# Kernel optimization log

Hardware: AMD Instinct MI355X
Metric: run time of the kernel (lower is better)

## Reference

```python
import jax, jax.numpy as jnp
import numpy as np

TAU = 0.5
LOGIT_TAU = float(np.log(TAU / (1.0 - TAU)))  # = 0.0 for tau=0.5
N_STEPS = 128           # torch samples randint(128,129) -> always 128
N_SECANT = 8
D_MIN, D_MAX = 0.0, 2.4
B, N, HID, CDIM = 4, 8192, 64, 128


def decoder(p, c, W1, Wc, b1, W2, b2):
    """Occupancy-logit MLP. p: (B, ..., 3), c: (B, CDIM) -> (B, ...)."""
    cc = c @ Wc  # (B, HID)
    cc = cc.reshape(cc.shape[:1] + (1,) * (p.ndim - 2) + cc.shape[1:])
    h = jax.nn.relu(jnp.einsum('...d,dh->...h', p, W1) + cc + b1)
    return (h @ W2 + b2)[..., 0]


def setup_inputs() -> dict:
    key = jax.random.key(0)
    ks = jax.random.split(key, 8)
    return {
        'ray0': jax.random.normal(ks[0], (B, N, 3), jnp.float32) * 0.5,
        'ray_direction': jax.random.normal(ks[1], (B, N, 3), jnp.float32),
        'c': jax.random.normal(ks[2], (B, CDIM), jnp.float32),
        'W1': jax.random.normal(ks[3], (3, HID), jnp.float32) * 0.5,
        'Wc': jax.random.normal(ks[4], (CDIM, HID), jnp.float32) * 0.1,
        'b1': jax.random.normal(ks[5], (HID,), jnp.float32) * 0.1,
        'W2': jax.random.normal(ks[6], (HID, 1), jnp.float32) * 0.5,
        'b2': jax.random.normal(ks[7], (1,), jnp.float32) * 0.1,
    }


def reference(ray0, ray_direction, c, W1, Wc, b1, W2, b2):
    S = N_STEPS
    bsz, npts, _ = ray0.shape
    dec = lambda p: decoder(p, c, W1, Wc, b1, W2, b2)

    # --- coarse ray marching ---
    d_prop = jnp.linspace(D_MIN, D_MAX, S).astype(ray0.dtype)        # (S,)
    p_prop = ray0[:, :, None, :] + ray_direction[:, :, None, :] * d_prop[None, None, :, None]
    val = dec(p_prop) - LOGIT_TAU                                    # (B, N, S)

    mask_0_not_occupied = val[:, :, 0] < 0
    sign_matrix = jnp.concatenate(
        [jnp.sign(val[:, :, :-1] * val[:, :, 1:]),
         jnp.ones((bsz, npts, 1), val.dtype)], axis=-1)
    cost_matrix = sign_matrix * jnp.arange(S, 0, -1, dtype=val.dtype)
    indices = jnp.argmin(cost_matrix, axis=-1)                       # (B, N)
    values = jnp.min(cost_matrix, axis=-1)
    mask_sign_change = values < 0
    f_low = jnp.take_along_axis(val, indices[..., None], axis=2)[..., 0]
    mask_neg_to_pos = f_low < 0
    mask = mask_sign_change & mask_neg_to_pos & mask_0_not_occupied

    d_prop_full = jnp.broadcast_to(d_prop, (bsz, npts, S))
    d_low = jnp.take_along_axis(d_prop_full, indices[..., None], axis=2)[..., 0]
    idx_hi = jnp.minimum(indices + 1, S - 1)
    d_high = jnp.take_along_axis(d_prop_full, idx_hi[..., None], axis=2)[..., 0]
    f_high = jnp.take_along_axis(val, idx_hi[..., None], axis=2)[..., 0]

    # safe placeholders for non-surface rays (results discarded by mask)
    d_low = jnp.where(mask, d_low, 0.0)
    d_high = jnp.where(mask, d_high, 1.0)
    f_low = jnp.where(mask, f_low, -1.0)
    f_high = jnp.where(mask, f_high, 1.0)

    # --- secant refinement (vectorized over all rays) ---
    d_pred = -f_low * (d_high - d_low) / (f_high - f_low) + d_low
    for _ in range(N_SECANT):
        p_mid = ray0 + d_pred[..., None] * ray_direction
        f_mid = dec(p_mid) - LOGIT_TAU
        ind_low = f_mid < 0
        d_low = jnp.where(ind_low, d_pred, d_low)
        f_low = jnp.where(ind_low, f_mid, f_low)
        d_high = jnp.where(ind_low, d_high, d_pred)
        f_high = jnp.where(ind_low, f_high, f_mid)
        d_pred = -f_low * (d_high - d_low) / (f_high - f_low) + d_low

    d_out = jnp.where(mask, d_pred, jnp.inf)
    d_out = jnp.where(mask_0_not_occupied, d_out, 0.0)
    return d_out
```

## Files before the change

### kernel.cpp

```cpp
#include <hip/hip_runtime.h>
#include <hip/hip_bf16.h>

#define HID   64
#define CDIM  128
#define NSTEP 128
#define NRAYS 32768

typedef const __hip_bfloat16* __restrict__ bf16p;
typedef float v2f __attribute__((ext_vector_type(2)));

__device__ __forceinline__ float bf2f(__hip_bfloat16 x) { return __bfloat162float(x); }

#if __has_builtin(__builtin_elementwise_fma)
__device__ __forceinline__ v2f vfma2(v2f a, v2f b, v2f c) { return __builtin_elementwise_fma(a, b, c); }
#else
__device__ __forceinline__ v2f vfma2(v2f a, v2f b, v2f c) {
    v2f r; r.x = fmaf(a.x, b.x, c.x); r.y = fmaf(a.y, b.y, c.y); return r;
}
#endif
#if __has_builtin(__builtin_elementwise_max)
__device__ __forceinline__ v2f vmax2(v2f a, v2f b) { return __builtin_elementwise_max(a, b); }
#else
__device__ __forceinline__ v2f vmax2(v2f a, v2f b) {
    v2f r; r.x = fmaxf(a.x, b.x); r.y = fmaxf(a.y, b.y); return r;
}
#endif
__device__ __forceinline__ v2f splat2(float s) { v2f v; v.x = s; v.y = s; return v; }

__global__ void precompute_cc(bf16p c, bf16p Wc, bf16p b1, float* __restrict__ ccb1) {
    __shared__ float part[4][HID];
    int b = blockIdx.x;
    int h = threadIdx.x & 63;
    int q = threadIdx.x >> 6;
    float acc = 0.0f;
    const __hip_bfloat16* crow = c + b * CDIM;
#pragma unroll
    for (int k = q * 32; k < q * 32 + 32; ++k)
        acc = fmaf(bf2f(crow[k]), bf2f(Wc[k * HID + h]), acc);
    part[q][h] = acc;
    __syncthreads();
    if (q == 0)
        ccb1[b * HID + h] = bf2f(b1[h]) + ((part[0][h] + part[1][h]) + (part[2][h] + part[3][h]));
}

__global__ __launch_bounds__(256) void raymarch(
    bf16p ray0, bf16p rdir, bf16p W1, bf16p W2, bf16p b2,
    const float* __restrict__ ccb1, __hip_bfloat16* __restrict__ out) {
    __shared__ float4 sWX[HID / 4], sWY[HID / 4], sWZ[HID / 4], sW2[HID / 4], sCB[HID / 4];

    const int tid  = threadIdx.x;
    const int wave = tid >> 6;
    const int lane = tid & 63;
    const int r    = blockIdx.x * 4 + wave;
    const int batch = blockIdx.x >> 11;

    if (tid < HID) {
        ((float*)sWX)[tid] = bf2f(W1[tid]);
        ((float*)sWY)[tid] = bf2f(W1[HID + tid]);
        ((float*)sWZ)[tid] = bf2f(W1[2 * HID + tid]);
        ((float*)sW2)[tid] = bf2f(W2[tid]);
        ((float*)sCB)[tid] = ccb1[batch * HID + tid];
    }
    __syncthreads();

    const float b2v = bf2f(b2[0]);
    const float ox = bf2f(ray0[r * 3 + 0]), oy = bf2f(ray0[r * 3 + 1]), oz = bf2f(ray0[r * 3 + 2]);
    const float dx = bf2f(rdir[r * 3 + 0]), dy = bf2f(rdir[r * 3 + 1]), dz = bf2f(rdir[r * 3 + 2]);

    const float STEPF = 2.4f / 127.0f;
    const float d0 = bf2f(__float2bfloat16(lane * STEPF));
    const float d1 = bf2f(__float2bfloat16((lane + 64) * STEPF));

    v2f dv; dv.x = d0; dv.y = d1;
    const v2f pxv = vfma2(dv, splat2(dx), splat2(ox));
    const v2f pyv = vfma2(dv, splat2(dy), splat2(oy));
    const v2f pzv = vfma2(dv, splat2(dz), splat2(oz));

    v2f acc = splat2(b2v);
    const v2f zero2 = splat2(0.0f);
#pragma unroll
    for (int g = 0; g < HID / 4; ++g) {
        const float4 wx4 = sWX[g], wy4 = sWY[g], wz4 = sWZ[g], w24 = sW2[g], cb4 = sCB[g];
        const float* wx = (const float*)&wx4;
        const float* wy = (const float*)&wy4;
        const float* wz = (const float*)&wz4;
        const float* w2 = (const float*)&w24;
        const float* cb = (const float*)&cb4;
#pragma unroll
        for (int jj = 0; jj < 4; ++jj) {
            v2f h = vfma2(pxv, splat2(wx[jj]),
                    vfma2(pyv, splat2(wy[jj]),
                    vfma2(pzv, splat2(wz[jj]), splat2(cb[jj]))));
            h = vmax2(h, zero2);
            acc = vfma2(h, splat2(w2[jj]), acc);
        }
    }
    float val0 = acc.x, val1 = acc.y;

    float v1l0  = __shfl(val1, 0);
    float valn0 = __shfl_down(val0, 1);
    valn0 = (lane == 63) ? v1l0 : valn0;
    float valn1 = __shfl_down(val1, 1);

    float prod0 = val0 * valn0;
    float sgn0  = (prod0 < 0.0f) ? -1.0f : ((prod0 > 0.0f) ? 1.0f : 0.0f);
    float cost0 = sgn0 * (float)(128 - lane);

    float prod1 = val1 * valn1;
    float sgn1  = (prod1 < 0.0f) ? -1.0f : ((prod1 > 0.0f) ? 1.0f : 0.0f);
    float cost1 = (lane == 63) ? 1.0f
                               : sgn1 * (float)(64 - lane);

    float key0 = fmaf(cost0, 256.0f, (float)lane);
    float key1 = fmaf(cost1, 256.0f, (float)(lane + 64));
    float k = fminf(key0, key1);
#pragma unroll
    for (int off = 32; off > 0; off >>= 1)
        k = fminf(k, __shfl_xor(k, off));
    const float cf = floorf(k * 0.00390625f);
    const int   mi = (int)(k - cf * 256.0f);

    const int idx  = mi;
    const int idxh = (idx + 1 < NSTEP) ? idx + 1 : NSTEP - 1;

    float va  = __shfl(val0, idx  & 63);
    float vb  = __shfl(val1, idx  & 63);
    float f_low  = (idx  < 64) ? va  : vb;
    float vah = __shfl(val0, idxh & 63);
    float vbh = __shfl(val1, idxh & 63);
    float f_high = (idxh < 64) ? vah : vbh;

    float v00 = __shfl(val0, 0);
    bool  m0   = v00 < 0.0f;
    bool  mask = (cf < 0.0f) && (f_low < 0.0f) && m0;

    float result;
    if (mask) {
        float dl = bf2f(__float2bfloat16(idx  * STEPF));
        float dh = bf2f(__float2bfloat16(idxh * STEPF));
        float fl = f_low, fh = f_high;
        const float wlx = ((const float*)sWX)[lane];
        const float wly = ((const float*)sWY)[lane];
        const float wlz = ((const float*)sWZ)[lane];
        const float wl2 = ((const float*)sW2)[lane];
        const float cbl = ((const float*)sCB)[lane];
        float dp = -fl * (dh - dl) / (fh - fl) + dl;
#pragma unroll
        for (int it = 0; it < 8; ++it) {
            float px = fmaf(dp, dx, ox), py = fmaf(dp, dy, oy), pz = fmaf(dp, dz, oz);
            float h = fmaf(px, wlx, fmaf(py, wly, fmaf(pz, wlz, cbl)));
            h = fmaxf(h, 0.0f);
            float t = h * wl2;
            for (int off = 32; off > 0; off >>= 1) t += __shfl_xor(t, off);
            float fm = t + b2v;
            bool lowside = fm < 0.0f;
            dl = lowside ? dp : dl;
            fl = lowside ? fm : fl;
            dh = lowside ? dh : dp;
            fh = lowside ? fh : fm;
            dp = -fl * (dh - dl) / (fh - fl) + dl;
        }
        result = dp;
    } else {
        result = m0 ? 0x1.FEp127f : 0.0f;
    }
    if (lane == 0) out[r] = __float2bfloat16(result);
}

extern "C" void kernel_launch(void* const* d_in, const int* in_sizes, int n_in,
                              void* d_out, int out_size, void* d_ws, size_t ws_size,
                              hipStream_t stream) {
    bf16p ray0 = (bf16p)d_in[0];
    bf16p rdir = (bf16p)d_in[1];
    bf16p c    = (bf16p)d_in[2];
    bf16p W1   = (bf16p)d_in[3];
    bf16p Wc   = (bf16p)d_in[4];
    bf16p b1   = (bf16p)d_in[5];
    bf16p W2   = (bf16p)d_in[6];
    bf16p b2   = (bf16p)d_in[7];
    __hip_bfloat16* out = (__hip_bfloat16*)d_out;
    float* ccb1 = (float*)d_ws;

    hipLaunchKernelGGL(precompute_cc, dim3(4), dim3(256), 0, stream, c, Wc, b1, ccb1);
    hipLaunchKernelGGL(raymarch, dim3(NRAYS / 4), dim3(256), 0, stream,
                       ray0, rdir, W1, W2, b2, ccb1, out);
}
```

Measured before the change: 100.4 us.

## Preconvert MLP weights to fp32 workspace and drop shared-memory staging

The precompute kernel now also converts W1 and W2 to fp32 in the workspace. The raymarch kernel reads weights directly from global memory (uniform, cacheable loads) instead of staging them in LDS behind a __syncthreads. The inner MLP loop is also restructured to vectorize over hidden units in pairs rather than over the two sample points, which needs a final horizontal add. This removes per-block bf16 conversion and the barrier, at the cost of relying on scalar/global cache loads for the weights.

```diff
diff --git a/kernel.cpp b/kernel.cpp
--- a/kernel.cpp
+++ b/kernel.cpp
@@ -8,6 +8,12 @@
 
 typedef const __hip_bfloat16* __restrict__ bf16p;
 typedef float v2f __attribute__((ext_vector_type(2)));
+
+#define WS_CCB 0
+#define WS_WX  256
+#define WS_WY  320
+#define WS_WZ  384
+#define WS_W2  448
 
 __device__ __forceinline__ float bf2f(__hip_bfloat16 x) { return __bfloat162float(x); }
 
@@ -27,7 +33,8 @@
 #endif
 __device__ __forceinline__ v2f splat2(float s) { v2f v; v.x = s; v.y = s; return v; }
 
-__global__ void precompute_cc(bf16p c, bf16p Wc, bf16p b1, float* __restrict__ ccb1) {
+__global__ void precompute_cc(bf16p c, bf16p Wc, bf16p b1, bf16p W1, bf16p W2,
+                              float* __restrict__ ws) {
     __shared__ float part[4][HID];
     int b = blockIdx.x;
     int h = threadIdx.x & 63;
@@ -38,30 +45,35 @@
     for (int k = q * 32; k < q * 32 + 32; ++k)
         acc = fmaf(bf2f(crow[k]), bf2f(Wc[k * HID + h]), acc);
     part[q][h] = acc;
+    if (b == 0) {
+        if (q == 1) {
+            ws[WS_WX + h] = bf2f(W1[h]);
+            ws[WS_WY + h] = bf2f(W1[HID + h]);
+        } else if (q == 2) {
+            ws[WS_WZ + h] = bf2f(W1[2 * HID + h]);
+            ws[WS_W2 + h] = bf2f(W2[h]);
+        }
+    }
     __syncthreads();
     if (q == 0)
-        ccb1[b * HID + h] = bf2f(b1[h]) + ((part[0][h] + part[1][h]) + (part[2][h] + part[3][h]));
+        ws[WS_CCB + b * HID + h] =
+            bf2f(b1[h]) + ((part[0][h] + part[1][h]) + (part[2][h] + part[3][h]));
 }
 
 __global__ __launch_bounds__(256) void raymarch(
-    bf16p ray0, bf16p rdir, bf16p W1, bf16p W2, bf16p b2,
-    const float* __restrict__ ccb1, __hip_bfloat16* __restrict__ out) {
-    __shared__ float4 sWX[HID / 4], sWY[HID / 4], sWZ[HID / 4], sW2[HID / 4], sCB[HID / 4];
-
+    bf16p ray0, bf16p rdir, bf16p b2,
+    const float* __restrict__ ws, __hip_bfloat16* __restrict__ out) {
     const int tid  = threadIdx.x;
     const int wave = tid >> 6;
     const int lane = tid & 63;
     const int r    = blockIdx.x * 4 + wave;
     const int batch = blockIdx.x >> 11;
 
-    if (tid < HID) {
-        ((float*)sWX)[tid] = bf2f(W1[tid]);
-        ((float*)sWY)[tid] = bf2f(W1[HID + tid]);
-        ((float*)sWZ)[tid] = bf2f(W1[2 * HID + tid]);
-        ((float*)sW2)[tid] = bf2f(W2[tid]);
-        ((float*)sCB)[tid] = ccb1[batch * HID + tid];
-    }
-    __syncthreads();
+    const float slx = ws[WS_WX + lane];
+    const float sly = ws[WS_WY + lane];
+    const float slz = ws[WS_WZ + lane];
+    const float sl2 = ws[WS_W2 + lane];
+    const float scb = ws[WS_CCB + batch * HID + lane];
 
     const float b2v = bf2f(b2[0]);
     const float ox = bf2f(ray0[r * 3 + 0]), oy = bf2f(ray0[r * 3 + 1]), oz = bf2f(ray0[r * 3 + 2]);
@@ -71,31 +83,33 @@
     const float d0 = bf2f(__float2bfloat16(lane * STEPF));
     const float d1 = bf2f(__float2bfloat16((lane + 64) * STEPF));
 
-    v2f dv; dv.x = d0; dv.y = d1;
-    const v2f pxv = vfma2(dv, splat2(dx), splat2(ox));
-    const v2f pyv = vfma2(dv, splat2(dy), splat2(oy));
-    const v2f pzv = vfma2(dv, splat2(dz), splat2(oz));
+    const float px0 = fmaf(d0, dx, ox), py0 = fmaf(d0, dy, oy), pz0 = fmaf(d0, dz, oz);
+    const float px1 = fmaf(d1, dx, ox), py1 = fmaf(d1, dy, oy), pz1 = fmaf(d1, dz, oz);
 
-    v2f acc = splat2(b2v);
+    const v2f px0v = splat2(px0), py0v = splat2(py0), pz0v = splat2(pz0);
+    const v2f px1v = splat2(px1), py1v = splat2(py1), pz1v = splat2(pz1);
     const v2f zero2 = splat2(0.0f);
-#pragma unroll
-    for (int g = 0; g < HID / 4; ++g) {
-        const float4 wx4 = sWX[g], wy4 = sWY[g], wz4 = sWZ[g], w24 = sW2[g], cb4 = sCB[g];
-        const float* wx = (const float*)&wx4;
-        const float* wy = (const float*)&wy4;
-        const float* wz = (const float*)&wz4;
-        const float* w2 = (const float*)&w24;
-        const float* cb = (const float*)&cb4;
-#pragma unroll
-        for (int jj = 0; jj < 4; ++jj) {
-            v2f h = vfma2(pxv, splat2(wx[jj]),
-                    vfma2(pyv, splat2(wy[jj]),
-                    vfma2(pzv, splat2(wz[jj]), splat2(cb[jj]))));
-            h = vmax2(h, zero2);
-            acc = vfma2(h, splat2(w2[jj]), acc);
-        }
+
+    const v2f* __restrict__ WX2 = (const v2f*)(ws + WS_WX);
+    const v2f* __restrict__ WY2 = (const v2f*)(ws + WS_WY);
+    const v2f* __restrict__ WZ2 = (const v2f*)(ws + WS_WZ);
+    const v2f* __restrict__ W22 = (const v2f*)(ws + WS_W2);
+    const v2f* __restrict__ CB2 = (const v2f*)(ws + WS_CCB + batch * HID);
+
+    v2f acc0; acc0.x = b2v; acc0.y = 0.0f;
+    v2f acc1 = acc0;
+#pragma unroll 8
+    for (int q = 0; q < HID / 2; ++q) {
+        const v2f wx = WX2[q], wy = WY2[q], wz = WZ2[q], w2 = W22[q], cb = CB2[q];
+        v2f h0 = vfma2(px0v, wx, vfma2(py0v, wy, vfma2(pz0v, wz, cb)));
+        v2f h1 = vfma2(px1v, wx, vfma2(py1v, wy, vfma2(pz1v, wz, cb)));
+        h0 = vmax2(h0, zero2);
+        h1 = vmax2(h1, zero2);
+        acc0 = vfma2(h0, w2, acc0);
+        acc1 = vfma2(h1, w2, acc1);
     }
-    float val0 = acc.x, val1 = acc.y;
+    float val0 = acc0.x + acc0.y;
+    float val1 = acc1.x + acc1.y;
 
     float v1l0  = __shfl(val1, 0);
     float valn0 = __shfl_down(val0, 1);
@@ -139,18 +153,13 @@
         float dl = bf2f(__float2bfloat16(idx  * STEPF));
         float dh = bf2f(__float2bfloat16(idxh * STEPF));
         float fl = f_low, fh = f_high;
-        const float wlx = ((const float*)sWX)[lane];
-        const float wly = ((const float*)sWY)[lane];
-        const float wlz = ((const float*)sWZ)[lane];
-        const float wl2 = ((const float*)sW2)[lane];
-        const float cbl = ((const float*)sCB)[lane];
         float dp = -fl * (dh - dl) / (fh - fl) + dl;
 #pragma unroll
         for (int it = 0; it < 8; ++it) {
             float px = fmaf(dp, dx, ox), py = fmaf(dp, dy, oy), pz = fmaf(dp, dz, oz);
-            float h = fmaf(px, wlx, fmaf(py, wly, fmaf(pz, wlz, cbl)));
+            float h = fmaf(px, slx, fmaf(py, sly, fmaf(pz, slz, scb)));
             h = fmaxf(h, 0.0f);
-            float t = h * wl2;
+            float t = h * sl2;
             for (int off = 32; off > 0; off >>= 1) t += __shfl_xor(t, off);
             float fm = t + b2v;
             bool lowside = fm < 0.0f;
@@ -179,9 +188,9 @@
     bf16p W2   = (bf16p)d_in[6];
     bf16p b2   = (bf16p)d_in[7];
     __hip_bfloat16* out = (__hip_bfloat16*)d_out;
-    float* ccb1 = (float*)d_ws;
+    float* ws = (float*)d_ws;
 
-    hipLaunchKernelGGL(precompute_cc, dim3(4), dim3(256), 0, stream, c, Wc, b1, ccb1);
+    hipLaunchKernelGGL(precompute_cc, dim3(4), dim3(256), 0, stream, c, Wc, b1, W1, W2, ws);
     hipLaunchKernelGGL(raymarch, dim3(NRAYS / 4), dim3(256), 0, stream,
-                       ray0, rdir, W1, W2, b2, ccb1, out);
+                       ray0, rdir, b2, ws, out);
 }
```

After: 99.58 us. No clear change (-0.8%).
